# Performance work log

Measured on AMD Instinct MI355X. Metric: run time of the kernel, lower is better.

## Reference

```python
import jax, jax.numpy as jnp
import numpy as np

B, S, D, H = 2, 2048, 1024, 16
DH = D // H


def setup_inputs() -> dict:
    key = jax.random.key(0)
    ks = jax.random.split(key, 12)
    f = lambda k, sh: jax.random.normal(k, sh, dtype=jnp.float32)
    inp = {"q": f(ks[0], (B, S, D)), "k": f(ks[1], (B, S, D)), "v": f(ks[2], (B, S, D))}
    scale = 1.0 / np.sqrt(D)
    names = ["q", "k", "v", "o"]
    for i, n in enumerate(names):
        inp["W" + n] = f(ks[3 + i], (D, D)) * scale
        inp["b" + n] = f(ks[7 + i], (D,)) * scale
    # causal mask: True = masked out
    inp["mask"] = jnp.triu(jnp.ones((S, S), dtype=bool), k=1)[None, None]
    return inp


def _rope(x):
    # x: [b, h, s, dh]; non-standard RoPE from AbsPositionEncoding
    s, dh = x.shape[2], x.shape[3]
    inv = jnp.exp(jnp.arange(0, dh, 2, dtype=jnp.float32) * (-(4.0 * jnp.log(jnp.float32(10.0))) / dh))
    pos = jnp.arange(s, dtype=jnp.float32)[:, None]
    sin = jnp.sin(pos * inv)  # [s, dh/2]
    cos = jnp.cos(pos * inv)
    x1 = x[..., 0::2]
    x2 = x[..., 1::2]
    out = jnp.stack([x1 * sin - x2 * cos, -x1 * cos - x2 * sin], axis=-1)
    return out.reshape(x.shape)


def reference(q, k, v, Wq, bq, Wk, bk, Wv, bv, Wo, bo, mask):
    b, s, d = q.shape
    h, dh = H, DH

    def proj(x, W, bias):
        return (x @ W.T + bias).reshape(b, -1, h, dh).transpose(0, 2, 1, 3)

    Q = proj(q, Wq, bq)
    K = proj(k, Wk, bk)
    V = proj(v, Wv, bv)
    PQ = _rope(Q)
    PK = _rope(K)
    # NOTE: source's forward() path applies NO 1/sqrt(dh) scaling
    scores = jnp.einsum('bhqd,bhkd->bhqk', PQ, PK)
    neg = jnp.finfo(scores.dtype).min
    scores = jnp.where(mask, neg, scores)
    p = jax.nn.softmax(scores, axis=-1)
    p = jnp.where(mask, jnp.float32(0.0), p)
    out = jnp.einsum('bhqk,bhkd->bhqd', p, V)
    out = out.transpose(0, 2, 1, 3).reshape(b, s, d)
    return out @ Wo.T + bo
```

## Files before the change

kernel.cpp:

```cpp
#include <hip/hip_runtime.h>
#include <stdint.h>

#define BB 2
#define SS 2048
#define DD 1024
#define HH 16
#define DH 64
#define MM 4096

typedef __attribute__((ext_vector_type(8))) short short8;
typedef __attribute__((ext_vector_type(4))) float floatx4;
typedef __attribute__((ext_vector_type(16))) float floatx16;
typedef unsigned short u16;

#define MFMA16(a,b,c) __builtin_amdgcn_mfma_f32_16x16x32_bf16((a),(b),(c),0,0,0)
#define MFMA32(a,b,c) __builtin_amdgcn_mfma_f32_32x32x16_bf16((a),(b),(c),0,0,0)

__device__ __forceinline__ u16 f2bf(float f) {
  unsigned u = __float_as_uint(f);
  u += 0x7fffu + ((u >> 16) & 1u);
  return (u16)(u >> 16);
}

__device__ __forceinline__ unsigned cvtpk(float lo, float hi2) {
  unsigned r;
  asm("v_cvt_pk_bf16_f32 %0, %1, %2" : "=v"(r) : "v"(lo), "v"(hi2));
  return r;
}

__device__ __forceinline__ void gll16(const void* g, void* l) {
  __builtin_amdgcn_global_load_lds((const __attribute__((address_space(1))) void*)g,
                                   (__attribute__((address_space(3))) void*)l,
                                   16, 0, 0);
}

__global__ __launch_bounds__(256) void prep(
    const float* __restrict__ q, const float* __restrict__ k, const float* __restrict__ v,
    const float* __restrict__ Wq, const float* __restrict__ Wk,
    const float* __restrict__ Wv, const float* __restrict__ Wo,
    u16* __restrict__ qb, u16* __restrict__ kb, u16* __restrict__ vb,
    u16* __restrict__ wqb, u16* __restrict__ wkb, u16* __restrict__ wvb, u16* __restrict__ wob,
    float2* __restrict__ tab) {
  int bid = blockIdx.x;
  if (bid < 256) {
    const int t = bid * 256 + threadIdx.x;
    const int s = t >> 5, j = t & 31;
    const float inv = expf(-(float)j * (0.125f * 2.302585092994046f));
    const float a = (float)s * inv;
    tab[t] = make_float2(sinf(a), cosf(a));
    return;
  }
  bid -= 256;
  const float* src;
  u16* dst;
  int x;
  if (bid < 12288) {
    const int z = bid >> 12;
    x = bid & 4095;
    src = z == 0 ? q : (z == 1 ? k : v);
    dst = z == 0 ? qb : (z == 1 ? kb : vb);
  } else {
    bid -= 12288;
    const int z = bid >> 10;
    x = bid & 1023;
    src = z == 0 ? Wq : (z == 1 ? Wk : (z == 2 ? Wv : Wo));
    dst = z == 0 ? wqb : (z == 1 ? wkb : (z == 2 ? wvb : wob));
  }
  const int i = (x * 256 + threadIdx.x) * 4;
  const float4 xv = *(const float4*)(src + i);
  ushort4 p; p.x = f2bf(xv.x); p.y = f2bf(xv.y); p.z = f2bf(xv.z); p.w = f2bf(xv.w);
  *(ushort4*)(dst + i) = p;
}

__device__ __forceinline__ void gemm_core128(const u16* __restrict__ A, const u16* __restrict__ Bt,
                                             int K, u16* As, u16* Bs, floatx4 acc[4][4],
                                             int m0, int n0) {
  const int tid = threadIdx.x;
  const int w = tid >> 6, l = tid & 63;
  const int lr = l & 15, lq = l >> 4;
  const int wm = (w >> 1) * 64, wn = (w & 1) * 64;

#pragma unroll
  for (int i = 0; i < 4; ++i)
#pragma unroll
    for (int j = 0; j < 4; ++j) acc[i][j] = (floatx4){0.f, 0.f, 0.f, 0.f};

  const int srow = w * 32 + (l >> 2);
  const int scol = (l & 3) * 8;
  const u16* ag = A + (size_t)(m0 + srow) * K + scol;
  const u16* bg = Bt + (size_t)(n0 + srow) * K + scol;
  u16* as0 = &As[w * 1024];
  u16* bs0 = &Bs[w * 1024];

  for (int k0 = 0; k0 < K; k0 += 32) {
    gll16(ag + k0, as0);
    gll16(ag + (size_t)16 * K + k0, as0 + 512);
    gll16(bg + k0, bs0);
    gll16(bg + (size_t)16 * K + k0, bs0 + 512);
    __syncthreads();
    short8 af[4], bfv[4];
#pragma unroll
    for (int i = 0; i < 4; ++i) af[i] = *(const short8*)&As[(wm + i * 16 + lr) * 32 + lq * 8];
#pragma unroll
    for (int j = 0; j < 4; ++j) bfv[j] = *(const short8*)&Bs[(wn + j * 16 + lr) * 32 + lq * 8];
    __builtin_amdgcn_s_setprio(1);
#pragma unroll
    for (int i = 0; i < 4; ++i)
#pragma unroll
      for (int j = 0; j < 4; ++j) acc[i][j] = MFMA16(af[i], bfv[j], acc[i][j]);
    __builtin_amdgcn_s_setprio(0);
    __syncthreads();
  }
}

__device__ __forceinline__ void gemm_core64(const u16* __restrict__ A, const u16* __restrict__ Bt,
                                            int K, u16* As, u16* Bs, floatx4 acc[2][4],
                                            int m0, int n0) {
  const int tid = threadIdx.x;
  const int w = tid >> 6, l = tid & 63;
  const int lr = l & 15, lq = l >> 4;
  const int wm = (w >> 1) * 32, wn = (w & 1) * 64;

#pragma unroll
  for (int i = 0; i < 2; ++i)
#pragma unroll
    for (int j = 0; j < 4; ++j) acc[i][j] = (floatx4){0.f, 0.f, 0.f, 0.f};

  const int arow = w * 16 + (l >> 2);
  const int brow = w * 32 + (l >> 2);
  const int scol = (l & 3) * 8;
  const u16* ag = A + (size_t)(m0 + arow) * K + scol;
  const u16* bg = Bt + (size_t)(n0 + brow) * K + scol;
  u16* as0 = &As[w * 512];
  u16* bs0 = &Bs[w * 1024];

  for (int k0 = 0; k0 < K; k0 += 32) {
    gll16(ag + k0, as0);
    gll16(bg + k0, bs0);
    gll16(bg + (size_t)16 * K + k0, bs0 + 512);
    __syncthreads();
    short8 af[2], bfv[4];
#pragma unroll
    for (int i = 0; i < 2; ++i) af[i] = *(const short8*)&As[(wm + i * 16 + lr) * 32 + lq * 8];
#pragma unroll
    for (int j = 0; j < 4; ++j) bfv[j] = *(const short8*)&Bs[(wn + j * 16 + lr) * 32 + lq * 8];
    __builtin_amdgcn_s_setprio(1);
#pragma unroll
    for (int i = 0; i < 2; ++i)
#pragma unroll
      for (int j = 0; j < 4; ++j) acc[i][j] = MFMA16(af[i], bfv[j], acc[i][j]);
    __builtin_amdgcn_s_setprio(0);
    __syncthreads();
  }
}

__global__ __launch_bounds__(256) void gemm3_fused(
    const u16* __restrict__ A0, const u16* __restrict__ A1, const u16* __restrict__ A2,
    const u16* __restrict__ B0, const u16* __restrict__ B1, const u16* __restrict__ B2,
    const float* __restrict__ c0, const float* __restrict__ c1, const float* __restrict__ c2,
    u16* __restrict__ Qro, u16* __restrict__ Kro, u16* __restrict__ Vtr,
    const float2* __restrict__ tab) {
  __shared__ alignas(16) u16 As[128 * 32];
  __shared__ alignas(16) u16 Bs[128 * 32];
  const int z = blockIdx.z;
  const u16* A = z == 0 ? A0 : (z == 1 ? A1 : A2);
  const u16* Bt = z == 0 ? B0 : (z == 1 ? B1 : B2);
  const float* bias = z == 0 ? c0 : (z == 1 ? c1 : c2);
  const int m0 = blockIdx.y * 128, n0 = blockIdx.x * 128;

  floatx4 acc[4][4];
  gemm_core128(A, Bt, DD, As, Bs, acc, m0, n0);

  const int tid = threadIdx.x;
  const int w = tid >> 6, l = tid & 63;
  const int lr = l & 15, lq = l >> 4;
  const int wm = (w >> 1) * 64, wn = (w & 1) * 64;

  if (z == 2) {
#pragma unroll
    for (int i = 0; i < 4; ++i) {
      const int row = m0 + wm + i * 16 + lq * 4;
      const int b = row >> 11, s = row & (SS - 1);
#pragma unroll
      for (int j = 0; j < 4; ++j) {
        const int col = n0 + wn + j * 16 + lr;
        const int h = col >> 6, e = col & 63;
        const float bv = bias[col];
        ushort4 pk;
        pk.x = f2bf(acc[i][j][0] + bv);
        pk.y = f2bf(acc[i][j][1] + bv);
        pk.z = f2bf(acc[i][j][2] + bv);
        pk.w = f2bf(acc[i][j][3] + bv);
        *(ushort4*)(Vtr + ((size_t)(b * HH + h) * DH + e) * SS + s) = pk;
      }
    }
  } else {
    u16* dst = z ? Kro : Qro;
#pragma unroll
    for (int i = 0; i < 4; ++i) {
#pragma unroll
      for (int j = 0; j < 4; ++j) {
        const int col = n0 + wn + j * 16 + lr;
        const int h = col >> 6, e = col & 63;
        const float bv = bias[col];
#pragma unroll
        for (int r = 0; r < 4; ++r) {
          const int row = m0 + wm + i * 16 + lq * 4 + r;
          const int b = row >> 11, s = row & (SS - 1);
          const float v = acc[i][j][r] + bv;
          const float p = __shfl_xor(v, 1);
          const float2 sc = tab[s * 32 + (e >> 1)];
          const float ov = ((e & 1) == 0) ? (v * sc.x - p * sc.y)
                                          : (-p * sc.y - v * sc.x);
          dst[((size_t)(b * HH + h) * SS + s) * DH + e] = f2bf(ov);
        }
      }
    }
  }
}

__global__ __launch_bounds__(256) void gemm_bt(const u16* __restrict__ A, const u16* __restrict__ Bt,
                                               const float* __restrict__ bias, float* __restrict__ C,
                                               int M, int N, int K) {
  __shared__ alignas(16) u16 As[64 * 32];
  __shared__ alignas(16) u16 Bs[128 * 32];
  const int m0 = blockIdx.y * 64, n0 = blockIdx.x * 128;
  floatx4 acc[2][4];
  gemm_core64(A, Bt, K, As, Bs, acc, m0, n0);

  const int tid = threadIdx.x;
  const int w = tid >> 6, l = tid & 63;
  const int lr = l & 15, lq = l >> 4;
  const int wm = (w >> 1) * 32, wn = (w & 1) * 64;
#pragma unroll
  for (int i = 0; i < 2; ++i) {
    const int row = m0 + wm + i * 16 + lq * 4;
#pragma unroll
    for (int j = 0; j < 4; ++j) {
      const int col = n0 + wn + j * 16 + lr;
      const float bv = bias[col];
      float* cp = C + (size_t)row * N + col;
#pragma unroll
      for (int r = 0; r < 4; ++r) cp[(size_t)r * N] = acc[i][j][r] + bv;
    }
  }
}

__global__ __launch_bounds__(64) void attn_fwd(const u16* __restrict__ Qr, const u16* __restrict__ Kr,
                                               const u16* __restrict__ Vt, u16* __restrict__ O) {
  __shared__ alignas(16) u16 Ks[2][32 * 64];
  __shared__ alignas(16) u16 Vs[2][64 * 32];
  const int bid = blockIdx.x;
  const int qi = 63 - (bid >> 5);
  const int bh = bid & 31;
  const int l = threadIdx.x;
  const int ql = l & 31, hi = l >> 5;
  const int qw0 = qi * 32;
  const u16* Qh = Qr + (size_t)bh * SS * DH;
  const u16* Kh = Kr + (size_t)bh * SS * DH;
  const u16* Vh = Vt + (size_t)bh * DH * SS;

  short8 qf[4];
#pragma unroll
  for (int i = 0; i < 4; ++i)
    qf[i] = *(const short8*)(Qh + (size_t)(qw0 + ql) * DH + i * 16 + hi * 8);

  floatx16 oacc[2];
#pragma unroll
  for (int dt = 0; dt < 2; ++dt)
#pragma unroll
    for (int r = 0; r < 16; ++r) oacc[dt][r] = 0.f;
  float mrun = -1e30f, lrun = 0.f;

  const int krow = l >> 3;
  const int kofs = ((((l & 7) * 16) ^ (((l >> 3) & 7) << 4)) >> 1);
  const int vrow = l >> 2;
  const int vofs = ((((l & 3) * 16) ^ (((l >> 2) & 3) << 4)) >> 1);
  const int swzk = (ql & 7) << 4;
  const int swzv = (ql & 3) << 4;

#define STAGE(buf, kv0)                                                              \
  do {                                                                               \
    gll16(Kh + (size_t)((kv0) + krow) * DH + kofs,      &Ks[buf][0 * 64]);           \
    gll16(Kh + (size_t)((kv0) + krow + 8) * DH + kofs,  &Ks[buf][8 * 64]);           \
    gll16(Kh + (size_t)((kv0) + krow + 16) * DH + kofs, &Ks[buf][16 * 64]);          \
    gll16(Kh + (size_t)((kv0) + krow + 24) * DH + kofs, &Ks[buf][24 * 64]);          \
    gll16(Vh + (size_t)vrow * SS + (kv0) + vofs,        &Vs[buf][0 * 32]);           \
    gll16(Vh + (size_t)(vrow + 16) * SS + (kv0) + vofs, &Vs[buf][16 * 32]);          \
    gll16(Vh + (size_t)(vrow + 32) * SS + (kv0) + vofs, &Vs[buf][32 * 32]);          \
    gll16(Vh + (size_t)(vrow + 48) * SS + (kv0) + vofs, &Vs[buf][48 * 32]);          \
  } while (0)

  const int T = qi + 1;
  STAGE(0, 0);
  asm volatile("s_waitcnt vmcnt(0)" ::: "memory");

  for (int t = 0; t < T; ++t) {
    const int cur = t & 1;
    if (t < T - 1) {
      STAGE(cur ^ 1, (t + 1) * 32);
      asm volatile("s_waitcnt vmcnt(8)" ::: "memory");
    } else {
      asm volatile("s_waitcnt vmcnt(0)" ::: "memory");
    }

    floatx16 st;
#pragma unroll
    for (int r = 0; r < 16; ++r) st[r] = 0.f;
    __builtin_amdgcn_s_setprio(1);
#pragma unroll
    for (int i = 0; i < 4; ++i) {
      const u16* kp = &Ks[cur][ql * 64 + (((32 * i + 16 * hi) ^ swzk) >> 1)];
      st = MFMA32(*(const short8*)kp, qf[i], st);
    }
    __builtin_amdgcn_s_setprio(0);

    if (t == T - 1) {
#pragma unroll
      for (int r = 0; r < 16; ++r) {
        const int kv = (r & 3) + 8 * (r >> 2) + 4 * hi;
        if (kv > ql) st[r] = -1e30f;
      }
    }

    float m8[8];
#pragma unroll
    for (int r = 0; r < 8; ++r) m8[r] = fmaxf(st[r], st[r + 8]);
    float m4a = fmaxf(m8[0], m8[4]), m4b = fmaxf(m8[1], m8[5]);
    float m4c = fmaxf(m8[2], m8[6]), m4d = fmaxf(m8[3], m8[7]);
    float tmax = fmaxf(fmaxf(m4a, m4b), fmaxf(m4c, m4d));
    tmax = fmaxf(tmax, __shfl_xor(tmax, 32));

    const float mn = fmaxf(mrun, tmax);
    const float sc = __expf(mrun - mn);
    mrun = mn;
    float ps = 0.f;
#pragma unroll
    for (int r = 0; r < 16; ++r) {
      const float p = __expf(st[r] - mn);
      st[r] = p;
      ps += p;
    }
    ps += __shfl_xor(ps, 32);
    lrun = lrun * sc + ps;
#pragma unroll
    for (int dt = 0; dt < 2; ++dt)
#pragma unroll
      for (int r = 0; r < 16; ++r) oacc[dt][r] *= sc;

    short8 pfrag[2];
#pragma unroll
    for (int c = 0; c < 2; ++c) {
      const int A0r = 2 * c, A1r = A0r + 1;
      const unsigned P00 = cvtpk(st[4 * A0r + 0], st[4 * A0r + 1]);
      const unsigned P01 = cvtpk(st[4 * A0r + 2], st[4 * A0r + 3]);
      const unsigned P10 = cvtpk(st[4 * A1r + 0], st[4 * A1r + 1]);
      const unsigned P11 = cvtpk(st[4 * A1r + 2], st[4 * A1r + 3]);
      const unsigned S0 = hi ? P00 : P10;
      const unsigned S1 = hi ? P01 : P11;
      const unsigned R0 = (unsigned)__shfl_xor((int)S0, 32);
      const unsigned R1 = (unsigned)__shfl_xor((int)S1, 32);
      union { unsigned u[4]; short8 s; } fd;
      fd.u[0] = hi ? R0 : P00;
      fd.u[1] = hi ? R1 : P01;
      fd.u[2] = hi ? P10 : R0;
      fd.u[3] = hi ? P11 : R1;
      pfrag[c] = fd.s;
    }

    __builtin_amdgcn_s_setprio(1);
#pragma unroll
    for (int dt = 0; dt < 2; ++dt)
#pragma unroll
      for (int c = 0; c < 2; ++c) {
        const u16* vp = &Vs[cur][(dt * 32 + ql) * 32 + (((32 * c + 16 * hi) ^ swzv) >> 1)];
        oacc[dt] = MFMA32(*(const short8*)vp, pfrag[c], oacc[dt]);
      }
    __builtin_amdgcn_s_setprio(0);
  }
#undef STAGE

  const float inv = 1.0f / lrun;
  const int b = bh >> 4, h = bh & 15;
  u16* orow = O + ((size_t)(b * SS + qw0 + ql)) * DD + h * DH;
#pragma unroll
  for (int dt = 0; dt < 2; ++dt)
#pragma unroll
    for (int g = 0; g < 4; ++g) {
      ushort4 pk;
      pk.x = f2bf(oacc[dt][4 * g + 0] * inv);
      pk.y = f2bf(oacc[dt][4 * g + 1] * inv);
      pk.z = f2bf(oacc[dt][4 * g + 2] * inv);
      pk.w = f2bf(oacc[dt][4 * g + 3] * inv);
      *(ushort4*)(orow + dt * 32 + 8 * g + 4 * hi) = pk;
    }
}

extern "C" void kernel_launch(void* const* d_in, const int* in_sizes, int n_in,
                              void* d_out, int out_size, void* d_ws, size_t ws_size,
                              hipStream_t stream) {
  (void)in_sizes; (void)n_in; (void)out_size; (void)ws_size;
  const float* q  = (const float*)d_in[0];
  const float* k  = (const float*)d_in[1];
  const float* v  = (const float*)d_in[2];
  const float* Wq = (const float*)d_in[3];
  const float* bq = (const float*)d_in[4];
  const float* Wk = (const float*)d_in[5];
  const float* bk = (const float*)d_in[6];
  const float* Wv = (const float*)d_in[7];
  const float* bv = (const float*)d_in[8];
  const float* Wo = (const float*)d_in[9];
  const float* bo = (const float*)d_in[10];
  float* out = (float*)d_out;

  char* ws = (char*)d_ws;
  size_t off = 0;
  auto carve = [&](size_t bytes) { char* p = ws + off; off += (bytes + 255) & ~(size_t)255; return p; };
  u16* qb   = (u16*)carve((size_t)MM * DD * 2);
  u16* kb   = (u16*)carve((size_t)MM * DD * 2);
  u16* vb   = (u16*)carve((size_t)MM * DD * 2);
  u16* wqb  = (u16*)carve((size_t)DD * DD * 2);
  u16* wkb  = (u16*)carve((size_t)DD * DD * 2);
  u16* wvb  = (u16*)carve((size_t)DD * DD * 2);
  u16* wob  = (u16*)carve((size_t)DD * DD * 2);
  u16* Qro  = (u16*)carve((size_t)MM * DD * 2);
  u16* Kro  = (u16*)carve((size_t)MM * DD * 2);
  u16* Vtr  = (u16*)carve((size_t)MM * DD * 2);
  float2* tab = (float2*)carve((size_t)SS * 32 * 8);
  u16* Ob = qb;

  prep<<<256 + 3 * 4096 + 4 * 1024, 256, 0, stream>>>(q, k, v, Wq, Wk, Wv, Wo,
                                                      qb, kb, vb, wqb, wkb, wvb, wob, tab);
  gemm3_fused<<<dim3(DD / 128, MM / 128, 3), 256, 0, stream>>>(qb, kb, vb, wqb, wkb, wvb,
                                                               bq, bk, bv, Qro, Kro, Vtr, tab);
  attn_fwd<<<64 * BB * HH, 64, 0, stream>>>(Qro, Kro, Vtr, Ob);
  gemm_bt<<<dim3(DD / 128, MM / 64), 256, 0, stream>>>(Ob, wob, bo, out, MM, DD, DD);
}
```

Measured before the change: 280.4 us.

## Load K and V fragments directly from global into registers in attention

```diff
diff --git a/kernel.cpp b/kernel.cpp
--- a/kernel.cpp
+++ b/kernel.cpp
@@ -248,8 +248,6 @@
 
 __global__ __launch_bounds__(64) void attn_fwd(const u16* __restrict__ Qr, const u16* __restrict__ Kr,
                                                const u16* __restrict__ Vt, u16* __restrict__ O) {
-  __shared__ alignas(16) u16 Ks[2][32 * 64];
-  __shared__ alignas(16) u16 Vs[2][64 * 32];
   const int bid = blockIdx.x;
   const int qi = 63 - (bid >> 5);
   const int bh = bid & 31;
@@ -272,113 +270,100 @@
     for (int r = 0; r < 16; ++r) oacc[dt][r] = 0.f;
   float mrun = -1e30f, lrun = 0.f;
 
-  const int krow = l >> 3;
-  const int kofs = ((((l & 7) * 16) ^ (((l >> 3) & 7) << 4)) >> 1);
-  const int vrow = l >> 2;
-  const int vofs = ((((l & 3) * 16) ^ (((l >> 2) & 3) << 4)) >> 1);
-  const int swzk = (ql & 7) << 4;
-  const int swzv = (ql & 3) << 4;
-
-#define STAGE(buf, kv0)                                                              \
+  const u16* kbase = Kh + (size_t)ql * DH + hi * 8;
+  const u16* vbase = Vh + (size_t)ql * SS + hi * 8;
+
+#define LOADK(kd, kv0)                                                      \
+  do {                                                                      \
+    const u16* kp_ = kbase + (size_t)(kv0) * DH;                            \
+    kd[0] = *(const short8*)(kp_);                                          \
+    kd[1] = *(const short8*)(kp_ + 16);                                     \
+    kd[2] = *(const short8*)(kp_ + 32);                                     \
+    kd[3] = *(const short8*)(kp_ + 48);                                     \
+  } while (0)
+
+#define COMPUTE(kd, tt)                                                              \
   do {                                                                               \
-    gll16(Kh + (size_t)((kv0) + krow) * DH + kofs,      &Ks[buf][0 * 64]);           \
-    gll16(Kh + (size_t)((kv0) + krow + 8) * DH + kofs,  &Ks[buf][8 * 64]);           \
-    gll16(Kh + (size_t)((kv0) + krow + 16) * DH + kofs, &Ks[buf][16 * 64]);          \
-    gll16(Kh + (size_t)((kv0) + krow + 24) * DH + kofs, &Ks[buf][24 * 64]);          \
-    gll16(Vh + (size_t)vrow * SS + (kv0) + vofs,        &Vs[buf][0 * 32]);           \
-    gll16(Vh + (size_t)(vrow + 16) * SS + (kv0) + vofs, &Vs[buf][16 * 32]);          \
-    gll16(Vh + (size_t)(vrow + 32) * SS + (kv0) + vofs, &Vs[buf][32 * 32]);          \
-    gll16(Vh + (size_t)(vrow + 48) * SS + (kv0) + vofs, &Vs[buf][48 * 32]);          \
+    const int kv0_ = (tt) * 32;                                                      \
+    floatx16 st;                                                                     \
+    _Pragma("unroll") for (int r = 0; r < 16; ++r) st[r] = 0.f;                      \
+    __builtin_amdgcn_s_setprio(1);                                                   \
+    _Pragma("unroll") for (int i = 0; i < 4; ++i) st = MFMA32(kd[i], qf[i], st);     \
+    __builtin_amdgcn_s_setprio(0);                                                   \
+    short8 vf[4];                                                                    \
+    {                                                                                \
+      const u16* vp_ = vbase + kv0_;                                                 \
+      vf[0] = *(const short8*)(vp_);                                                 \
+      vf[1] = *(const short8*)(vp_ + 16);                                            \
+      vf[2] = *(const short8*)(vp_ + (size_t)32 * SS);                               \
+      vf[3] = *(const short8*)(vp_ + (size_t)32 * SS + 16);                          \
+    }                                                                                \
+    if ((tt) == T - 1) {                             \
+      _Pragma("unroll") for (int r = 0; r < 16; ++r) {                               \
+        const int kv = (r & 3) + 8 * (r >> 2) + 4 * hi;                              \
+        if (kv > ql) st[r] = -1e30f;                                                 \
+      }                                                                              \
+    }                                                                                \
+    float m8[8];                                                                     \
+    _Pragma("unroll") for (int r = 0; r < 8; ++r) m8[r] = fmaxf(st[r], st[r + 8]);   \
+    float m4a = fmaxf(m8[0], m8[4]), m4b = fmaxf(m8[1], m8[5]);                      \
+    float m4c = fmaxf(m8[2], m8[6]), m4d = fmaxf(m8[3], m8[7]);                      \
+    float tmax = fmaxf(fmaxf(m4a, m4b), fmaxf(m4c, m4d));                            \
+    tmax = fmaxf(tmax, __shfl_xor(tmax, 32));                                        \
+    const float mn = fmaxf(mrun, tmax);                                              \
+    const float sc = __expf(mrun - mn);                                              \
+    mrun = mn;                                                                       \
+    float ps = 0.f;                                                                  \
+    _Pragma("unroll") for (int r = 0; r < 16; ++r) {                                 \
+      const float p = __expf(st[r] - mn);                                            \
+      st[r] = p;                                                                     \
+      ps += p;                                                                       \
+    }                                                                                \
+    ps += __shfl_xor(ps, 32);                                                        \
+    lrun = lrun * sc + ps;                                                           \
+    _Pragma("unroll") for (int dt = 0; dt < 2; ++dt)                                 \
+      _Pragma("unroll") for (int r = 0; r < 16; ++r) oacc[dt][r] *= sc;              \
+    short8 pfrag[2];                                                                 \
+    _Pragma("unroll") for (int c = 0; c < 2; ++c) {                                  \
+      const int A0r = 2 * c, A1r = A0r + 1;                                          \
+      const unsigned P00 = cvtpk(st[4 * A0r + 0], st[4 * A0r + 1]);                  \
+      const unsigned P01 = cvtpk(st[4 * A0r + 2], st[4 * A0r + 3]);                  \
+      const unsigned P10 = cvtpk(st[4 * A1r + 0], st[4 * A1r + 1]);                  \
+      const unsigned P11 = cvtpk(st[4 * A1r + 2], st[4 * A1r + 3]);                  \
+      const unsigned S0 = hi ? P00 : P10;                                            \
+      const unsigned S1 = hi ? P01 : P11;                                            \
+      const unsigned R0 = (unsigned)__shfl_xor((int)S0, 32);                         \
+      const unsigned R1 = (unsigned)__shfl_xor((int)S1, 32);                         \
+      union { unsigned u[4]; short8 s; } fd;                                         \
+      fd.u[0] = hi ? R0 : P00;                                                       \
+      fd.u[1] = hi ? R1 : P01;                                                       \
+      fd.u[2] = hi ? P10 : R0;                                                       \
+      fd.u[3] = hi ? P11 : R1;                                                       \
+      pfrag[c] = fd.s;                                                               \
+    }                                                                                \
+    __builtin_amdgcn_s_setprio(1);                                                   \
+    _Pragma("unroll") for (int dt = 0; dt < 2; ++dt)                                 \
+      _Pragma("unroll") for (int c = 0; c < 2; ++c)                                  \
+        oacc[dt] = MFMA32(vf[dt * 2 + c], pfrag[c], oacc[dt]);                       \
+    __builtin_amdgcn_s_setprio(0);                                                   \
   } while (0)
 
   const int T = qi + 1;
-  STAGE(0, 0);
-  asm volatile("s_waitcnt vmcnt(0)" ::: "memory");
-
-  for (int t = 0; t < T; ++t) {
-    const int cur = t & 1;
-    if (t < T - 1) {
-      STAGE(cur ^ 1, (t + 1) * 32);
-      asm volatile("s_waitcnt vmcnt(8)" ::: "memory");
-    } else {
-      asm volatile("s_waitcnt vmcnt(0)" ::: "memory");
-    }
-
-    floatx16 st;
-#pragma unroll
-    for (int r = 0; r < 16; ++r) st[r] = 0.f;
-    __builtin_amdgcn_s_setprio(1);
-#pragma unroll
-    for (int i = 0; i < 4; ++i) {
-      const u16* kp = &Ks[cur][ql * 64 + (((32 * i + 16 * hi) ^ swzk) >> 1)];
-      st = MFMA32(*(const short8*)kp, qf[i], st);
-    }
-    __builtin_amdgcn_s_setprio(0);
-
-    if (t == T - 1) {
-#pragma unroll
-      for (int r = 0; r < 16; ++r) {
-        const int kv = (r & 3) + 8 * (r >> 2) + 4 * hi;
-        if (kv > ql) st[r] = -1e30f;
-      }
-    }
-
-    float m8[8];
-#pragma unroll
-    for (int r = 0; r < 8; ++r) m8[r] = fmaxf(st[r], st[r + 8]);
-    float m4a = fmaxf(m8[0], m8[4]), m4b = fmaxf(m8[1], m8[5]);
-    float m4c = fmaxf(m8[2], m8[6]), m4d = fmaxf(m8[3], m8[7]);
-    float tmax = fmaxf(fmaxf(m4a, m4b), fmaxf(m4c, m4d));
-    tmax = fmaxf(tmax, __shfl_xor(tmax, 32));
-
-    const float mn = fmaxf(mrun, tmax);
-    const float sc = __expf(mrun - mn);
-    mrun = mn;
-    float ps = 0.f;
-#pragma unroll
-    for (int r = 0; r < 16; ++r) {
-      const float p = __expf(st[r] - mn);
-      st[r] = p;
-      ps += p;
-    }
-    ps += __shfl_xor(ps, 32);
-    lrun = lrun * sc + ps;
-#pragma unroll
-    for (int dt = 0; dt < 2; ++dt)
-#pragma unroll
-      for (int r = 0; r < 16; ++r) oacc[dt][r] *= sc;
-
-    short8 pfrag[2];
-#pragma unroll
-    for (int c = 0; c < 2; ++c) {
-      const int A0r = 2 * c, A1r = A0r + 1;
-      const unsigned P00 = cvtpk(st[4 * A0r + 0], st[4 * A0r + 1]);
-      const unsigned P01 = cvtpk(st[4 * A0r + 2], st[4 * A0r + 3]);
-      const unsigned P10 = cvtpk(st[4 * A1r + 0], st[4 * A1r + 1]);
-      const unsigned P11 = cvtpk(st[4 * A1r + 2], st[4 * A1r + 3]);
-      const unsigned S0 = hi ? P00 : P10;
-      const unsigned S1 = hi ? P01 : P11;
-      const unsigned R0 = (unsigned)__shfl_xor((int)S0, 32);
-      const unsigned R1 = (unsigned)__shfl_xor((int)S1, 32);
-      union { unsigned u[4]; short8 s; } fd;
-      fd.u[0] = hi ? R0 : P00;
-      fd.u[1] = hi ? R1 : P01;
-      fd.u[2] = hi ? P10 : R0;
-      fd.u[3] = hi ? P11 : R1;
-      pfrag[c] = fd.s;
-    }
-
-    __builtin_amdgcn_s_setprio(1);
-#pragma unroll
-    for (int dt = 0; dt < 2; ++dt)
-#pragma unroll
-      for (int c = 0; c < 2; ++c) {
-        const u16* vp = &Vs[cur][(dt * 32 + ql) * 32 + (((32 * c + 16 * hi) ^ swzv) >> 1)];
-        oacc[dt] = MFMA32(*(const short8*)vp, pfrag[c], oacc[dt]);
-      }
-    __builtin_amdgcn_s_setprio(0);
-  }
-#undef STAGE
+  short8 kA[4], kB[4];
+  LOADK(kA, 0);
+  int t = 0;
+  while (true) {
+    if (t + 1 < T) LOADK(kB, (t + 1) * 32);
+    COMPUTE(kA, t);
+    ++t;
+    if (t >= T) break;
+    if (t + 1 < T) LOADK(kA, (t + 1) * 32);
+    COMPUTE(kB, t);
+    ++t;
+    if (t >= T) break;
+  }
+#undef COMPUTE
+#undef LOADK
 
   const float inv = 1.0f / lrun;
   const int b = bh >> 4, h = bh & 15;
```

Result: no change. 282.3 us (+0.7%).
